# Optimization experiments

Hardware: AMD Instinct MI355X
Metric: run time of the kernel (lower is better)

## Reference

```python
import jax, jax.numpy as jnp
import numpy as np

B, S, H, I, E, K = 2, 1024, 768, 1536, 8, 2
CAPACITY_FACTOR = 1.5
ROUTING_TEMP = 1.0
LB_WEIGHT = 0.001


def setup_inputs() -> dict:
    key = jax.random.key(0)
    k_x, k_g, k_w1, k_w3, k_w2 = jax.random.split(key, 5)
    std = 0.02
    return {
        "x": jax.random.normal(k_x, (B, S, H), dtype=jnp.float32),
        "w_gate": jax.random.normal(k_g, (H, E), dtype=jnp.float32) * 0.02,
        "w1": jax.random.normal(k_w1, (E, H, I), dtype=jnp.float32) * std,
        "w3": jax.random.normal(k_w3, (E, H, I), dtype=jnp.float32) * std,
        "w2": jax.random.normal(k_w2, (E, I, H), dtype=jnp.float32) * (std / np.sqrt(2 * 12)),
    }


def _moe_forward(x, w_gate, w1, w3, w2):
    Bb, Ss, Hh = x.shape
    T = Bb * Ss
    xf = x.reshape(T, Hh)

    # --- routing ---
    gate_logits = (xf @ w_gate) / ROUTING_TEMP          # [T, E]
    gate_probs = jax.nn.softmax(gate_logits, axis=-1)   # [T, E]
    topk_probs, topk_idx = jax.lax.top_k(gate_probs, K)  # [T, K]
    topk_probs = topk_probs / (topk_probs.sum(-1, keepdims=True) + 1e-8)

    # --- capacity dropping (per-k slot, token order, like the torch loop) ---
    capacity = max(8, int((T * K // E) * CAPACITY_FACTOR))
    onehot = (topk_idx[:, :, None] == jnp.arange(E)[None, None, :])  # [T, K, E] bool
    ranks = jnp.cumsum(onehot.astype(jnp.int32), axis=0)             # position of token in expert queue
    keep = onehot & (ranks <= capacity)                               # [T, K, E]

    # combine weight per (token, expert): sum over k of kept, clamped routing prob
    w_clamped = jnp.clip(topk_probs, 1e-8, 10.0)                      # [T, K]
    combine = jnp.einsum("tk,tke->te", w_clamped, keep.astype(xf.dtype))  # [T, E]

    # --- dense per-expert SwiGLU (reference form of masked dispatch) ---
    g = jnp.einsum("th,ehi->tei", xf, w1)   # [T, E, I]
    u = jnp.einsum("th,ehi->tei", xf, w3)   # [T, E, I]
    h = jax.nn.silu(g) * u                    # [T, E, I]
    y = jnp.einsum("tei,eih->teh", h, w2)   # [T, E, H]
    out = jnp.einsum("te,teh->th", combine, y).reshape(Bb, Ss, Hh)

    # --- load balancing loss ---
    expert_counts = keep.sum(axis=(0, 1)).astype(jnp.float32)         # [E]
    dropped = (onehot.sum() - keep.sum()).astype(jnp.float32)
    expert_usage = jax.lax.stop_gradient(expert_counts) / float(max(T * K, 1))
    gate_importance = gate_probs.mean(axis=0)                          # [E]
    aux = jnp.sum(expert_usage * gate_importance) * E
    aux = aux + jnp.where(dropped > 0, dropped / float(max(T, 1)) * 0.1, 0.0)
    aux = jnp.minimum(aux, 1.0) * LB_WEIGHT
    return out, aux


def reference(x, w_gate, w1, w3, w2):
    return _moe_forward(x, w_gate, w1, w3, w2)
```

## Files before the change

### kernel.cpp

```cpp
#include <hip/hip_runtime.h>
#include <math.h>

#define T_TOK 2048
#define HD 768
#define ID 1536
#define NE 8
#define CAP 768
#define TK 4096
#define RT 12
#define NB1 24
#define KC1 24
#define NB2 12
#define KC2 48

typedef __bf16 bf16_t;
typedef __bf16 bf16x8 __attribute__((ext_vector_type(8)));
typedef __bf16 bf16x4 __attribute__((ext_vector_type(4)));
typedef float floatx4 __attribute__((ext_vector_type(4)));

__device__ __forceinline__ void gld16(const bf16_t* g, bf16_t* l) {
  __builtin_amdgcn_global_load_lds(
      (__attribute__((address_space(1))) void*)(g),
      (__attribute__((address_space(3))) void*)(l),
      16, 0, 0);
}

__global__ void k_prep(const float* __restrict__ x, const float* __restrict__ wg,
                       const float* __restrict__ w1, const float* __restrict__ w3,
                       const float* __restrict__ w2,
                       bf16_t* __restrict__ xbf, bf16_t* __restrict__ w1b,
                       bf16_t* __restrict__ w3b, bf16_t* __restrict__ w2b,
                       int2* __restrict__ idx2, float2* __restrict__ wc2,
                       float* __restrict__ probs8, float* __restrict__ outz) {
  int b = blockIdx.x;
  int tid = threadIdx.x;
  if (b < 512) {
#pragma unroll
    for (int k2 = 0; k2 < 3; ++k2) {
      float4 z = make_float4(0.f, 0.f, 0.f, 0.f);
      *(float4*)(outz + (size_t)b * 3072 + k2 * 1024 + tid * 4) = z;
    }
    int t = b * 4 + (tid >> 6);
    int lane = tid & 63;
    const float* xr = x + (size_t)t * HD;
    int off = lane * 12;
    float4 a = *(const float4*)(xr + off);
    float4 bv = *(const float4*)(xr + off + 4);
    float4 c = *(const float4*)(xr + off + 8);
    float xv[12] = {a.x, a.y, a.z, a.w, bv.x, bv.y, bv.z, bv.w, c.x, c.y, c.z, c.w};
    bf16x4 s0, s1, s2;
#pragma unroll
    for (int j = 0; j < 4; ++j) { s0[j] = (bf16_t)xv[j]; s1[j] = (bf16_t)xv[4 + j]; s2[j] = (bf16_t)xv[8 + j]; }
    bf16_t* xo = xbf + (size_t)t * HD + off;
    *(bf16x4*)xo = s0; *(bf16x4*)(xo + 4) = s1; *(bf16x4*)(xo + 8) = s2;

    float acc[8] = {0, 0, 0, 0, 0, 0, 0, 0};
#pragma unroll
    for (int jj = 0; jj < 12; ++jj) {
      const float4* wr = (const float4*)(wg + (size_t)(off + jj) * 8);
      float4 w0 = wr[0], w1v = wr[1];
      float v = xv[jj];
      acc[0] += v * w0.x; acc[1] += v * w0.y; acc[2] += v * w0.z; acc[3] += v * w0.w;
      acc[4] += v * w1v.x; acc[5] += v * w1v.y; acc[6] += v * w1v.z; acc[7] += v * w1v.w;
    }
#pragma unroll
    for (int e = 0; e < 8; ++e) {
      float v = acc[e];
      for (int s = 1; s < 64; s <<= 1) v += __shfl_xor(v, s, 64);
      acc[e] = v;
    }
    float mx = acc[0];
#pragma unroll
    for (int e = 1; e < 8; ++e) mx = fmaxf(mx, acc[e]);
    float p[8], sum = 0.f;
#pragma unroll
    for (int e = 0; e < 8; ++e) { p[e] = __expf(acc[e] - mx); sum += p[e]; }
#pragma unroll
    for (int e = 0; e < 8; ++e) p[e] /= sum;
    if (lane == 0) {
      float4 P0 = make_float4(p[0], p[1], p[2], p[3]);
      float4 P1 = make_float4(p[4], p[5], p[6], p[7]);
      *(float4*)&probs8[t * 8] = P0;
      *(float4*)&probs8[t * 8 + 4] = P1;
      int e0 = 0;
#pragma unroll
      for (int e = 1; e < 8; ++e) if (p[e] > p[e0]) e0 = e;
      int e1 = (e0 == 0) ? 1 : 0;
#pragma unroll
      for (int e = 0; e < 8; ++e) if (e != e0 && p[e] > p[e1]) e1 = e;
      float denom = p[e0] + p[e1] + 1e-8f;
      float w0c = fminf(fmaxf(p[e0] / denom, 1e-8f), 10.f);
      float w1c = fminf(fmaxf(p[e1] / denom, 1e-8f), 10.f);
      idx2[t] = make_int2(e0, e1);
      wc2[t] = make_float2(w0c, w1c);
    }
  } else {
    int rb = b - 512;
    const float* src; bf16_t* dst; int C; int kc0;
    if (rb < 1152) {
      int m = rb >= 576;
      int r3 = m ? rb - 576 : rb;
      int pan = r3 / 3;
      kc0 = (r3 - pan * 3) * 8;
      int e = pan & 7, nb = pan >> 3;
      src = (m ? w3 : w1) + (size_t)e * HD * ID + nb * 64;
      dst = (m ? w3b : w1b) + (size_t)(e * NB1 + nb) * (KC1 * 2048);
      C = ID;
    } else {
      int q = rb - 1152;
      int pan = q / 6;
      kc0 = (q - pan * 6) * 8;
      int e = pan & 7, nb = pan >> 3;
      src = w2 + (size_t)e * ID * HD + nb * 64;
      dst = w2b + (size_t)(e * NB2 + nb) * (KC2 * 2048);
      C = HD;
    }
    int n = tid >> 2, p4 = tid & 3;
    int c8 = p4 ^ ((n >> 1) & 3);
    const float* sp0 = src + n + (size_t)(kc0 * 32 + c8 * 8) * C;
    bf16_t* dp = dst + (size_t)kc0 * 2048 + tid * 8;
#pragma unroll 2
    for (int t = 0; t < 8; ++t) {
      const float* sp = sp0 + (size_t)t * 32 * C;
      float v[8];
#pragma unroll
      for (int j = 0; j < 8; ++j) v[j] = sp[(size_t)j * C];
      bf16x8 o;
#pragma unroll
      for (int j = 0; j < 8; ++j) o[j] = (bf16_t)v[j];
      *(bf16x8*)(dp + t * 2048) = o;
    }
  }
}

__global__ void k_scan(const int2* __restrict__ idx2, const float2* __restrict__ wc2,
                       const float* __restrict__ probs8,
                       int* __restrict__ tok_of_row, float* __restrict__ wgt_of_row,
                       int2* __restrict__ cnt_start, float* __restrict__ aux_out) {
  __shared__ int2 sIdx[2048];
  __shared__ float2 sWc[2048];
  __shared__ int sTot[16];
  __shared__ int sPos[8];
  __shared__ float sImp[16][8];
  int tid = threadIdx.x;
  sIdx[tid] = idx2[tid]; sIdx[tid + 1024] = idx2[tid + 1024];
  sWc[tid] = wc2[tid];  sWc[tid + 1024] = wc2[tid + 1024];
  const float4* pp = (const float4*)probs8;
  float4 u0 = pp[tid * 4], u1 = pp[tid * 4 + 1], u2 = pp[tid * 4 + 2], u3 = pp[tid * 4 + 3];
  float im[8] = {u0.x + u2.x, u0.y + u2.y, u0.z + u2.z, u0.w + u2.w,
                 u1.x + u3.x, u1.y + u3.y, u1.z + u3.z, u1.w + u3.w};
#pragma unroll
  for (int e = 0; e < 8; ++e) {
    float v = im[e];
    for (int d = 1; d < 64; d <<= 1) v += __shfl_xor(v, d, 64);
    im[e] = v;
  }
  int w = tid >> 6, lane = tid & 63;
  if (lane == 0) {
#pragma unroll
    for (int e = 0; e < 8; ++e) sImp[w][e] = im[e];
  }
  __syncthreads();
  int s = w >> 3, e = w & 7;
  int t0 = lane * 32;
  int cnt = 0;
  for (int j = 0; j < 32; ++j) {
    int2 p = sIdx[t0 + j];
    cnt += ((s ? p.y : p.x) == e) ? 1 : 0;
  }
  int incl = cnt;
  for (int d = 1; d < 64; d <<= 1) {
    int v = __shfl_up(incl, d, 64);
    if (lane >= d) incl += v;
  }
  int excl = incl - cnt;
  if (lane == 63) sTot[w] = incl;
  __syncthreads();
  if (tid == 0) {
    int run = 0; float a = 0.f;
    for (int ee = 0; ee < 8; ++ee) {
      float impv = 0.f;
      for (int ww = 0; ww < 16; ++ww) impv += sImp[ww][ee];
      int k = min(sTot[ee], CAP) + min(sTot[8 + ee], CAP);
      sPos[ee] = run;
      cnt_start[ee] = make_int2(run, k);
      a += ((float)k / (float)TK) * (impv / (float)T_TOK);
      run += k;
    }
    a *= (float)NE;
    int dropped = TK - run;
    if (dropped > 0) a += (float)dropped / (float)T_TOK * 0.1f;
    aux_out[0] = fminf(a, 1.f) * 0.001f;
  }
  __syncthreads();
  int rank = excl;
  for (int j = 0; j < 32; ++j) {
    int t = t0 + j;
    int2 p = sIdx[t];
    int ex = s ? p.y : p.x;
    if (ex == e) {
      rank++;
      if (rank <= CAP) {
        int pos = atomicAdd(&sPos[e], 1);
        tok_of_row[pos] = t;
        float2 wv = sWc[t];
        wgt_of_row[pos] = s ? wv.y : wv.x;
      }
    }
  }
}

__global__ __launch_bounds__(256, 4)
void k_gemm1(const bf16_t* __restrict__ xbf, const bf16_t* __restrict__ w1b,
             const bf16_t* __restrict__ w3b, const int* __restrict__ tok_of_row,
             const int2* __restrict__ cnt_start, bf16_t* __restrict__ h_ws) {
  int e = blockIdx.x & 7;
  int t = blockIdx.x >> 3;
  int nb = t / RT, rt = t - nb * RT;
  int2 cs = cnt_start[e];
  int nrows = cs.y - rt * 128;
  if (nrows <= 0) return;
  if (nrows > 128) nrows = 128;
  int grow0 = cs.x + rt * 128;

  __shared__ __attribute__((aligned(16))) bf16_t Abuf[128 * 32];
  __shared__ __attribute__((aligned(16))) bf16_t B1buf[64 * 32];
  __shared__ __attribute__((aligned(16))) bf16_t B3buf[64 * 32];

  int tid = threadIdx.x;
  int lane = tid & 63, wv = tid >> 6;
  int wm = wv & 1, wn = wv >> 1;
  int lr = lane & 15, q = lane >> 4;
  int rdc = (q ^ ((lane >> 1) & 3)) * 8;
  int srow = lane >> 2;
  int gch = ((lane & 3) ^ ((lane >> 3) & 3)) * 8;

  int ra = wv * 32 + srow;
  int tokA0 = tok_of_row[grow0 + min(ra, nrows - 1)];
  int tokA1 = tok_of_row[grow0 + min(ra + 16, nrows - 1)];
  const bf16_t* gA0 = xbf + (size_t)tokA0 * HD + gch;
  const bf16_t* gA1 = xbf + (size_t)tokA1 * HD + gch;
  const bf16_t* p1 = w1b + (size_t)((e * NB1 + nb) * KC1) * 2048 + tid * 8;
  const bf16_t* p3 = w3b + (size_t)((e * NB1 + nb) * KC1) * 2048 + tid * 8;
  bf16_t* lA0 = &Abuf[(wv * 32) * 32];
  bf16_t* lA1 = &Abuf[(wv * 32 + 16) * 32];
  bf16_t* lB1 = &B1buf[wv * 512];
  bf16_t* lB3 = &B3buf[wv * 512];

  floatx4 accg[4][2] = {};
  floatx4 accu[4][2] = {};

  for (int kk = 0; kk < KC1; ++kk) {
    __syncthreads();
    gld16(gA0, lA0); gld16(gA1, lA1);
    gld16(p1, lB1); gld16(p3, lB3);
    gA0 += 32; gA1 += 32; p1 += 2048; p3 += 2048;
    __syncthreads();
    bf16x8 af[4], b1f[2], b3f[2];
#pragma unroll
    for (int i = 0; i < 4; ++i) af[i] = *(const bf16x8*)&Abuf[(wm * 64 + i * 16 + lr) * 32 + rdc];
#pragma unroll
    for (int i = 0; i < 2; ++i) b1f[i] = *(const bf16x8*)&B1buf[(wn * 32 + i * 16 + lr) * 32 + rdc];
#pragma unroll
    for (int i = 0; i < 2; ++i) b3f[i] = *(const bf16x8*)&B3buf[(wn * 32 + i * 16 + lr) * 32 + rdc];
#pragma unroll
    for (int i = 0; i < 4; ++i)
#pragma unroll
      for (int jj = 0; jj < 2; ++jj) {
        accg[i][jj] = __builtin_amdgcn_mfma_f32_16x16x32_bf16(af[i], b1f[jj], accg[i][jj], 0, 0, 0);
        accu[i][jj] = __builtin_amdgcn_mfma_f32_16x16x32_bf16(af[i], b3f[jj], accu[i][jj], 0, 0, 0);
      }
  }
#pragma unroll
  for (int i = 0; i < 4; ++i)
#pragma unroll
    for (int r = 0; r < 4; ++r) {
      int rl = wm * 64 + i * 16 + q * 4 + r;
      if (rl < nrows) {
        size_t rb = (size_t)(grow0 + rl) * ID + nb * 64 + wn * 32 + lr;
#pragma unroll
        for (int jj = 0; jj < 2; ++jj) {
          float gg = accg[i][jj][r], uu = accu[i][jj][r];
          float sg = gg / (1.f + __expf(-gg));
          h_ws[rb + jj * 16] = (bf16_t)(sg * uu);
        }
      }
    }
}

__global__ __launch_bounds__(256, 4)
void k_gemm2(const bf16_t* __restrict__ h_ws, const bf16_t* __restrict__ w2b,
             const int* __restrict__ tok_of_row, const float* __restrict__ wgt_of_row,
             const int2* __restrict__ cnt_start, float* __restrict__ out) {
  int e = blockIdx.x & 7;
  int t = blockIdx.x >> 3;
  int nb = t / RT, rt = t - nb * RT;
  int2 cs = cnt_start[e];
  int nrows = cs.y - rt * 128;
  if (nrows <= 0) return;
  if (nrows > 128) nrows = 128;
  int grow0 = cs.x + rt * 128;

  __shared__ __attribute__((aligned(16))) bf16_t Abuf[128 * 32];
  __shared__ __attribute__((aligned(16))) bf16_t Bbuf[64 * 32];

  int tid = threadIdx.x;
  int lane = tid & 63, wv = tid >> 6;
  int wm = wv & 1, wn = wv >> 1;
  int lr = lane & 15, q = lane >> 4;
  int rdc = (q ^ ((lane >> 1) & 3)) * 8;
  int srow = lane >> 2;
  int gch = ((lane & 3) ^ ((lane >> 3) & 3)) * 8;

  int ra = wv * 32 + srow;
  const bf16_t* gA0 = h_ws + (size_t)(grow0 + min(ra, nrows - 1)) * ID + gch;
  const bf16_t* gA1 = h_ws + (size_t)(grow0 + min(ra + 16, nrows - 1)) * ID + gch;
  const bf16_t* pB = w2b + (size_t)((e * NB2 + nb) * KC2) * 2048 + tid * 8;
  bf16_t* lA0 = &Abuf[(wv * 32) * 32];
  bf16_t* lA1 = &Abuf[(wv * 32 + 16) * 32];
  bf16_t* lB = &Bbuf[wv * 512];

  floatx4 acc[4][2] = {};

  for (int kk = 0; kk < KC2; ++kk) {
    __syncthreads();
    gld16(gA0, lA0); gld16(gA1, lA1);
    gld16(pB, lB);
    gA0 += 32; gA1 += 32; pB += 2048;
    __syncthreads();
    bf16x8 af[4], bfr[2];
#pragma unroll
    for (int i = 0; i < 4; ++i) af[i] = *(const bf16x8*)&Abuf[(wm * 64 + i * 16 + lr) * 32 + rdc];
#pragma unroll
    for (int i = 0; i < 2; ++i) bfr[i] = *(const bf16x8*)&Bbuf[(wn * 32 + i * 16 + lr) * 32 + rdc];
#pragma unroll
    for (int i = 0; i < 4; ++i)
#pragma unroll
      for (int jj = 0; jj < 2; ++jj)
        acc[i][jj] = __builtin_amdgcn_mfma_f32_16x16x32_bf16(af[i], bfr[jj], acc[i][jj], 0, 0, 0);
  }
#pragma unroll
  for (int i = 0; i < 4; ++i)
#pragma unroll
    for (int r = 0; r < 4; ++r) {
      int rl = wm * 64 + i * 16 + q * 4 + r;
      if (rl < nrows) {
        int grow = grow0 + rl;
        int tok = tok_of_row[grow];
        float wgt = wgt_of_row[grow];
        size_t ob = (size_t)tok * HD + nb * 64 + wn * 32 + lr;
#pragma unroll
        for (int jj = 0; jj < 2; ++jj)
          atomicAdd(&out[ob + jj * 16], wgt * acc[i][jj][r]);
      }
    }
}

extern "C" void kernel_launch(void* const* d_in, const int* in_sizes, int n_in,
                              void* d_out, int out_size, void* d_ws, size_t ws_size,
                              hipStream_t stream) {
  const float* x  = (const float*)d_in[0];
  const float* wg = (const float*)d_in[1];
  const float* w1 = (const float*)d_in[2];
  const float* w3 = (const float*)d_in[3];
  const float* w2 = (const float*)d_in[4];
  float* out = (float*)d_out;

  char* ws = (char*)d_ws;
  bf16_t* xbf  = (bf16_t*)(ws + 0);
  bf16_t* w1b  = (bf16_t*)(ws + 3145728);
  bf16_t* w3b  = (bf16_t*)(ws + 22020096);
  bf16_t* w2b  = (bf16_t*)(ws + 40894464);
  bf16_t* h_ws = (bf16_t*)(ws + 59768832);
  float*  probs8     = (float*)(ws + 72351744);
  int2*   idx2       = (int2*)(ws + 72417280);
  float2* wc2        = (float2*)(ws + 72433664);
  int*    tok_of_row = (int*)(ws + 72450048);
  float*  wgt_of_row = (float*)(ws + 72466432);
  int2*   cnt_start  = (int2*)(ws + 72482816);

  float* aux_out = out + (size_t)T_TOK * HD;

  k_prep<<<2240, 256, 0, stream>>>(x, wg, w1, w3, w2, xbf, w1b, w3b, w2b,
                                   idx2, wc2, probs8, out);
  k_scan<<<1, 1024, 0, stream>>>(idx2, wc2, probs8, tok_of_row, wgt_of_row,
                                 cnt_start, aux_out);
  k_gemm1<<<8 * NB1 * RT, 256, 0, stream>>>(xbf, w1b, w3b, tok_of_row,
                                            cnt_start, h_ws);
  k_gemm2<<<8 * NB2 * RT, 256, 0, stream>>>(h_ws, w2b, tok_of_row, wgt_of_row,
                                            cnt_start, out);
}
```

Before: 261.8 us.

## Overlap weight repacking with scan and gemm1, replace atomic scatter with combine kernel

```diff
diff --git a/kernel.cpp b/kernel.cpp
--- a/kernel.cpp
+++ b/kernel.cpp
@@ -12,6 +12,7 @@
 #define KC1 24
 #define NB2 12
 #define KC2 48
+#define W2BLK 576
 
 typedef __bf16 bf16_t;
 typedef __bf16 bf16x8 __attribute__((ext_vector_type(8)));
@@ -25,126 +26,135 @@
       16, 0, 0);
 }
 
-__global__ void k_prep(const float* __restrict__ x, const float* __restrict__ wg,
-                       const float* __restrict__ w1, const float* __restrict__ w3,
-                       const float* __restrict__ w2,
-                       bf16_t* __restrict__ xbf, bf16_t* __restrict__ w1b,
-                       bf16_t* __restrict__ w3b, bf16_t* __restrict__ w2b,
-                       int2* __restrict__ idx2, float2* __restrict__ wc2,
-                       float* __restrict__ probs8, float* __restrict__ outz) {
+__device__ __forceinline__ void repack_unit256(const float* __restrict__ src,
+                                               bf16_t* __restrict__ dst, int C,
+                                               int kc0, int tid) {
+  int n = tid >> 2, p4 = tid & 3;
+  int c8 = p4 ^ ((n >> 1) & 3);
+  const float* sp0 = src + n + (size_t)(kc0 * 32 + c8 * 8) * C;
+  bf16_t* dp = dst + (size_t)kc0 * 2048 + tid * 8;
+#pragma unroll 2
+  for (int t = 0; t < 8; ++t) {
+    const float* sp = sp0 + (size_t)t * 32 * C;
+    float v[8];
+#pragma unroll
+    for (int j = 0; j < 8; ++j) v[j] = sp[(size_t)j * C];
+    bf16x8 o;
+#pragma unroll
+    for (int j = 0; j < 8; ++j) o[j] = (bf16_t)v[j];
+    *(bf16x8*)(dp + t * 2048) = o;
+  }
+}
+
+__device__ __forceinline__ void repack_unit1024(const float* __restrict__ src,
+                                                bf16_t* __restrict__ dst, int C,
+                                                int kc0, int tid1024) {
+  int tid = tid1024 & 255;
+  int tq = tid1024 >> 8;
+  int n = tid >> 2, p4 = tid & 3;
+  int c8 = p4 ^ ((n >> 1) & 3);
+  const float* sp0 = src + n + (size_t)(kc0 * 32 + c8 * 8) * C;
+  bf16_t* dp = dst + (size_t)kc0 * 2048 + tid * 8;
+#pragma unroll
+  for (int tt = 0; tt < 2; ++tt) {
+    int t = tq * 2 + tt;
+    const float* sp = sp0 + (size_t)t * 32 * C;
+    float v[8];
+#pragma unroll
+    for (int j = 0; j < 8; ++j) v[j] = sp[(size_t)j * C];
+    bf16x8 o;
+#pragma unroll
+    for (int j = 0; j < 8; ++j) o[j] = (bf16_t)v[j];
+    *(bf16x8*)(dp + t * 2048) = o;
+  }
+}
+
+__global__ void k_route(const float* __restrict__ x, const float* __restrict__ wg,
+                        bf16_t* __restrict__ xbf, int2* __restrict__ idx2,
+                        float2* __restrict__ wc2, float* __restrict__ probs8) {
   int b = blockIdx.x;
   int tid = threadIdx.x;
-  if (b < 512) {
-#pragma unroll
-    for (int k2 = 0; k2 < 3; ++k2) {
-      float4 z = make_float4(0.f, 0.f, 0.f, 0.f);
-      *(float4*)(outz + (size_t)b * 3072 + k2 * 1024 + tid * 4) = z;
-    }
-    int t = b * 4 + (tid >> 6);
-    int lane = tid & 63;
-    const float* xr = x + (size_t)t * HD;
-    int off = lane * 12;
-    float4 a = *(const float4*)(xr + off);
-    float4 bv = *(const float4*)(xr + off + 4);
-    float4 c = *(const float4*)(xr + off + 8);
-    float xv[12] = {a.x, a.y, a.z, a.w, bv.x, bv.y, bv.z, bv.w, c.x, c.y, c.z, c.w};
-    bf16x4 s0, s1, s2;
-#pragma unroll
-    for (int j = 0; j < 4; ++j) { s0[j] = (bf16_t)xv[j]; s1[j] = (bf16_t)xv[4 + j]; s2[j] = (bf16_t)xv[8 + j]; }
-    bf16_t* xo = xbf + (size_t)t * HD + off;
-    *(bf16x4*)xo = s0; *(bf16x4*)(xo + 4) = s1; *(bf16x4*)(xo + 8) = s2;
-
-    float acc[8] = {0, 0, 0, 0, 0, 0, 0, 0};
-#pragma unroll
-    for (int jj = 0; jj < 12; ++jj) {
-      const float4* wr = (const float4*)(wg + (size_t)(off + jj) * 8);
-      float4 w0 = wr[0], w1v = wr[1];
-      float v = xv[jj];
-      acc[0] += v * w0.x; acc[1] += v * w0.y; acc[2] += v * w0.z; acc[3] += v * w0.w;
-      acc[4] += v * w1v.x; acc[5] += v * w1v.y; acc[6] += v * w1v.z; acc[7] += v * w1v.w;
-    }
-#pragma unroll
-    for (int e = 0; e < 8; ++e) {
-      float v = acc[e];
-      for (int s = 1; s < 64; s <<= 1) v += __shfl_xor(v, s, 64);
-      acc[e] = v;
-    }
-    float mx = acc[0];
-#pragma unroll
-    for (int e = 1; e < 8; ++e) mx = fmaxf(mx, acc[e]);
-    float p[8], sum = 0.f;
-#pragma unroll
-    for (int e = 0; e < 8; ++e) { p[e] = __expf(acc[e] - mx); sum += p[e]; }
-#pragma unroll
-    for (int e = 0; e < 8; ++e) p[e] /= sum;
-    if (lane == 0) {
-      float4 P0 = make_float4(p[0], p[1], p[2], p[3]);
-      float4 P1 = make_float4(p[4], p[5], p[6], p[7]);
-      *(float4*)&probs8[t * 8] = P0;
-      *(float4*)&probs8[t * 8 + 4] = P1;
-      int e0 = 0;
-#pragma unroll
-      for (int e = 1; e < 8; ++e) if (p[e] > p[e0]) e0 = e;
-      int e1 = (e0 == 0) ? 1 : 0;
-#pragma unroll
-      for (int e = 0; e < 8; ++e) if (e != e0 && p[e] > p[e1]) e1 = e;
-      float denom = p[e0] + p[e1] + 1e-8f;
-      float w0c = fminf(fmaxf(p[e0] / denom, 1e-8f), 10.f);
-      float w1c = fminf(fmaxf(p[e1] / denom, 1e-8f), 10.f);
-      idx2[t] = make_int2(e0, e1);
-      wc2[t] = make_float2(w0c, w1c);
-    }
-  } else {
-    int rb = b - 512;
-    const float* src; bf16_t* dst; int C; int kc0;
-    if (rb < 1152) {
-      int m = rb >= 576;
-      int r3 = m ? rb - 576 : rb;
-      int pan = r3 / 3;
-      kc0 = (r3 - pan * 3) * 8;
-      int e = pan & 7, nb = pan >> 3;
-      src = (m ? w3 : w1) + (size_t)e * HD * ID + nb * 64;
-      dst = (m ? w3b : w1b) + (size_t)(e * NB1 + nb) * (KC1 * 2048);
-      C = ID;
-    } else {
-      int q = rb - 1152;
-      int pan = q / 6;
-      kc0 = (q - pan * 6) * 8;
-      int e = pan & 7, nb = pan >> 3;
-      src = w2 + (size_t)e * ID * HD + nb * 64;
-      dst = w2b + (size_t)(e * NB2 + nb) * (KC2 * 2048);
-      C = HD;
-    }
-    int n = tid >> 2, p4 = tid & 3;
-    int c8 = p4 ^ ((n >> 1) & 3);
-    const float* sp0 = src + n + (size_t)(kc0 * 32 + c8 * 8) * C;
-    bf16_t* dp = dst + (size_t)kc0 * 2048 + tid * 8;
-#pragma unroll 2
-    for (int t = 0; t < 8; ++t) {
-      const float* sp = sp0 + (size_t)t * 32 * C;
-      float v[8];
-#pragma unroll
-      for (int j = 0; j < 8; ++j) v[j] = sp[(size_t)j * C];
-      bf16x8 o;
-#pragma unroll
-      for (int j = 0; j < 8; ++j) o[j] = (bf16_t)v[j];
-      *(bf16x8*)(dp + t * 2048) = o;
-    }
+  int t = b * 4 + (tid >> 6);
+  int lane = tid & 63;
+  const float* xr = x + (size_t)t * HD;
+  int off = lane * 12;
+  float4 a = *(const float4*)(xr + off);
+  float4 bv = *(const float4*)(xr + off + 4);
+  float4 c = *(const float4*)(xr + off + 8);
+  float xv[12] = {a.x, a.y, a.z, a.w, bv.x, bv.y, bv.z, bv.w, c.x, c.y, c.z, c.w};
+  bf16x4 s0, s1, s2;
+#pragma unroll
+  for (int j = 0; j < 4; ++j) { s0[j] = (bf16_t)xv[j]; s1[j] = (bf16_t)xv[4 + j]; s2[j] = (bf16_t)xv[8 + j]; }
+  bf16_t* xo = xbf + (size_t)t * HD + off;
+  *(bf16x4*)xo = s0; *(bf16x4*)(xo + 4) = s1; *(bf16x4*)(xo + 8) = s2;
+
+  float acc[8] = {0, 0, 0, 0, 0, 0, 0, 0};
+#pragma unroll
+  for (int jj = 0; jj < 12; ++jj) {
+    const float4* wr = (const float4*)(wg + (size_t)(off + jj) * 8);
+    float4 w0 = wr[0], w1v = wr[1];
+    float v = xv[jj];
+    acc[0] += v * w0.x; acc[1] += v * w0.y; acc[2] += v * w0.z; acc[3] += v * w0.w;
+    acc[4] += v * w1v.x; acc[5] += v * w1v.y; acc[6] += v * w1v.z; acc[7] += v * w1v.w;
+  }
+#pragma unroll
+  for (int e = 0; e < 8; ++e) {
+    float v = acc[e];
+    for (int s = 1; s < 64; s <<= 1) v += __shfl_xor(v, s, 64);
+    acc[e] = v;
+  }
+  float mx = acc[0];
+#pragma unroll
+  for (int e = 1; e < 8; ++e) mx = fmaxf(mx, acc[e]);
+  float p[8], sum = 0.f;
+#pragma unroll
+  for (int e = 0; e < 8; ++e) { p[e] = __expf(acc[e] - mx); sum += p[e]; }
+#pragma unroll
+  for (int e = 0; e < 8; ++e) p[e] /= sum;
+  if (lane == 0) {
+    float4 P0 = make_float4(p[0], p[1], p[2], p[3]);
+    float4 P1 = make_float4(p[4], p[5], p[6], p[7]);
+    *(float4*)&probs8[t * 8] = P0;
+    *(float4*)&probs8[t * 8 + 4] = P1;
+    int e0 = 0;
+#pragma unroll
+    for (int e = 1; e < 8; ++e) if (p[e] > p[e0]) e0 = e;
+    int e1 = (e0 == 0) ? 1 : 0;
+#pragma unroll
+    for (int e = 0; e < 8; ++e) if (e != e0 && p[e] > p[e1]) e1 = e;
+    float denom = p[e0] + p[e1] + 1e-8f;
+    float w0c = fminf(fmaxf(p[e0] / denom, 1e-8f), 10.f);
+    float w1c = fminf(fmaxf(p[e1] / denom, 1e-8f), 10.f);
+    idx2[t] = make_int2(e0, e1);
+    wc2[t] = make_float2(w0c, w1c);
   }
 }
 
 __global__ void k_scan(const int2* __restrict__ idx2, const float2* __restrict__ wc2,
                        const float* __restrict__ probs8,
-                       int* __restrict__ tok_of_row, float* __restrict__ wgt_of_row,
+                       const float* __restrict__ w1, const float* __restrict__ w3,
+                       bf16_t* __restrict__ w1b, bf16_t* __restrict__ w3b,
+                       int* __restrict__ tok_of_row, int2* __restrict__ rows2,
                        int2* __restrict__ cnt_start, float* __restrict__ aux_out) {
+  if (blockIdx.x > 0) {
+    int rb = blockIdx.x - 1;
+    int m = rb >= 576;
+    int r3 = m ? rb - 576 : rb;
+    int pan = r3 / 3;
+    int kc0 = (r3 - pan * 3) * 8;
+    int e = pan & 7, nb = pan >> 3;
+    const float* src = (m ? w3 : w1) + (size_t)e * HD * ID + nb * 64;
+    bf16_t* dst = (m ? w3b : w1b) + (size_t)(e * NB1 + nb) * (KC1 * 2048);
+    repack_unit1024(src, dst, ID, kc0, threadIdx.x);
+    return;
+  }
   __shared__ int2 sIdx[2048];
-  __shared__ float2 sWc[2048];
   __shared__ int sTot[16];
   __shared__ int sPos[8];
   __shared__ float sImp[16][8];
   int tid = threadIdx.x;
   sIdx[tid] = idx2[tid]; sIdx[tid + 1024] = idx2[tid + 1024];
-  sWc[tid] = wc2[tid];  sWc[tid + 1024] = wc2[tid + 1024];
+  rows2[tid] = make_int2(-1, -1); rows2[tid + 1024] = make_int2(-1, -1);
   const float4* pp = (const float4*)probs8;
   float4 u0 = pp[tid * 4], u1 = pp[tid * 4 + 1], u2 = pp[tid * 4 + 2], u3 = pp[tid * 4 + 3];
   float im[8] = {u0.x + u2.x, u0.y + u2.y, u0.z + u2.z, u0.w + u2.w,
@@ -203,8 +213,7 @@
       if (rank <= CAP) {
         int pos = atomicAdd(&sPos[e], 1);
         tok_of_row[pos] = t;
-        float2 wv = sWc[t];
-        wgt_of_row[pos] = s ? wv.y : wv.x;
+        ((int*)rows2)[2 * t + s] = pos;
       }
     }
   }
@@ -212,10 +221,22 @@
 
 __global__ __launch_bounds__(256, 4)
 void k_gemm1(const bf16_t* __restrict__ xbf, const bf16_t* __restrict__ w1b,
-             const bf16_t* __restrict__ w3b, const int* __restrict__ tok_of_row,
+             const bf16_t* __restrict__ w3b, const float* __restrict__ w2,
+             bf16_t* __restrict__ w2b, const int* __restrict__ tok_of_row,
              const int2* __restrict__ cnt_start, bf16_t* __restrict__ h_ws) {
-  int e = blockIdx.x & 7;
-  int t = blockIdx.x >> 3;
+  if (blockIdx.x < W2BLK) {
+    int q = blockIdx.x;
+    int pan = q / 6;
+    int kc0 = (q - pan * 6) * 8;
+    int e = pan & 7, nb = pan >> 3;
+    const float* src = w2 + (size_t)e * ID * HD + nb * 64;
+    bf16_t* dst = w2b + (size_t)(e * NB2 + nb) * (KC2 * 2048);
+    repack_unit256(src, dst, HD, kc0, threadIdx.x);
+    return;
+  }
+  int bx = blockIdx.x - W2BLK;
+  int e = bx & 7;
+  int t = bx >> 3;
   int nb = t / RT, rt = t - nb * RT;
   int2 cs = cnt_start[e];
   int nrows = cs.y - rt * 128;
@@ -290,8 +311,7 @@
 
 __global__ __launch_bounds__(256, 4)
 void k_gemm2(const bf16_t* __restrict__ h_ws, const bf16_t* __restrict__ w2b,
-             const int* __restrict__ tok_of_row, const float* __restrict__ wgt_of_row,
-             const int2* __restrict__ cnt_start, float* __restrict__ out) {
+             const int2* __restrict__ cnt_start, float* __restrict__ y) {
   int e = blockIdx.x & 7;
   int t = blockIdx.x >> 3;
   int nb = t / RT, rt = t - nb * RT;
@@ -345,15 +365,41 @@
     for (int r = 0; r < 4; ++r) {
       int rl = wm * 64 + i * 16 + q * 4 + r;
       if (rl < nrows) {
-        int grow = grow0 + rl;
-        int tok = tok_of_row[grow];
-        float wgt = wgt_of_row[grow];
-        size_t ob = (size_t)tok * HD + nb * 64 + wn * 32 + lr;
+        size_t ob = (size_t)(grow0 + rl) * HD + nb * 64 + wn * 32 + lr;
 #pragma unroll
         for (int jj = 0; jj < 2; ++jj)
-          atomicAdd(&out[ob + jj * 16], wgt * acc[i][jj][r]);
+          y[ob + jj * 16] = acc[i][jj][r];
       }
     }
+}
+
+__global__ void k_comb(const float* __restrict__ y, const int2* __restrict__ rows2,
+                       const float2* __restrict__ wc2, float* __restrict__ out) {
+  int tid = threadIdx.x;
+  int t = blockIdx.x * 4 + (tid >> 6);
+  int lane = tid & 63;
+  int2 r = rows2[t];
+  float2 w = wc2[t];
+  int off = lane * 12;
+  floatx4 o0 = {0.f, 0.f, 0.f, 0.f}, o1 = o0, o2 = o0;
+  if (r.x >= 0) {
+    const float* yr = y + (size_t)r.x * HD + off;
+    floatx4 a = *(const floatx4*)(yr);
+    floatx4 b = *(const floatx4*)(yr + 4);
+    floatx4 c = *(const floatx4*)(yr + 8);
+    o0 += w.x * a; o1 += w.x * b; o2 += w.x * c;
+  }
+  if (r.y >= 0) {
+    const float* yr = y + (size_t)r.y * HD + off;
+    floatx4 a = *(const floatx4*)(yr);
+    floatx4 b = *(const floatx4*)(yr + 4);
+    floatx4 c = *(const floatx4*)(yr + 8);
+    o0 += w.y * a; o1 += w.y * b; o2 += w.y * c;
+  }
+  float* op = out + (size_t)t * HD + off;
+  *(floatx4*)(op) = o0;
+  *(floatx4*)(op + 4) = o1;
+  *(floatx4*)(op + 8) = o2;
 }
 
 extern "C" void kernel_launch(void* const* d_in, const int* in_sizes, int n_in,
@@ -376,17 +422,17 @@
   int2*   idx2       = (int2*)(ws + 72417280);
   float2* wc2        = (float2*)(ws + 72433664);
   int*    tok_of_row = (int*)(ws + 72450048);
-  float*  wgt_of_row = (float*)(ws + 72466432);
+  int2*   rows2      = (int2*)(ws + 72466432);
   int2*   cnt_start  = (int2*)(ws + 72482816);
+  float*  y_ws = (float*)(ws + 3145728);
 
   float* aux_out = out + (size_t)T_TOK * HD;
 
-  k_prep<<<2240, 256, 0, stream>>>(x, wg, w1, w3, w2, xbf, w1b, w3b, w2b,
-                                   idx2, wc2, probs8, out);
-  k_scan<<<1, 1024, 0, stream>>>(idx2, wc2, probs8, tok_of_row, wgt_of_row,
-                                 cnt_start, aux_out);
-  k_gemm1<<<8 * NB1 * RT, 256, 0, stream>>>(xbf, w1b, w3b, tok_of_row,
-                                            cnt_start, h_ws);
-  k_gemm2<<<8 * NB2 * RT, 256, 0, stream>>>(h_ws, w2b, tok_of_row, wgt_of_row,
-                                            cnt_start, out);
-}
+  k_route<<<512, 256, 0, stream>>>(x, wg, xbf, idx2, wc2, probs8);
+  k_scan<<<1 + 1152, 1024, 0, stream>>>(idx2, wc2, probs8, w1, w3, w1b, w3b,
+                                        tok_of_row, rows2, cnt_start, aux_out);
+  k_gemm1<<<W2BLK + 8 * NB1 * RT, 256, 0, stream>>>(xbf, w1b, w3b, w2, w2b,
+                                                    tok_of_row, cnt_start, h_ws);
+  k_gemm2<<<8 * NB2 * RT, 256, 0, stream>>>(h_ws, w2b, cnt_start, y_ws);
+  k_comb<<<512, 256, 0, stream>>>(y_ws, rows2, wc2, out);
+}
```

Result: faster. 235.5 us (-10.1%).

## Coalesce weight repack via LDS transpose and fuse routing scan into GEMM1

Applied to the files above, without the earlier changes.

```diff
diff --git a/kernel.cpp b/kernel.cpp
--- a/kernel.cpp
+++ b/kernel.cpp
@@ -25,16 +25,68 @@
       16, 0, 0);
 }
 
+__device__ __forceinline__ unsigned short bfbits(float f) {
+  union { bf16_t b; unsigned short u; } c;
+  c.b = (bf16_t)f;
+  return c.u;
+}
+
+__device__ __forceinline__ void rp_load(const float* __restrict__ src, int C,
+                                        int kc, int t256, unsigned* T32) {
+  int r = t256 >> 3, c0 = (t256 & 7) * 8;
+  const float* sp = src + (size_t)(kc * 32 + r) * C + c0;
+  float4 v0 = *(const float4*)sp;
+  float4 v1 = *(const float4*)(sp + 4);
+  float f[8] = {v0.x, v0.y, v0.z, v0.w, v1.x, v1.y, v1.z, v1.w};
+  unsigned* tb = T32 + r * 33 + (c0 >> 1);
+#pragma unroll
+  for (int k = 0; k < 4; ++k)
+    tb[k] = (unsigned)bfbits(f[2 * k]) | ((unsigned)bfbits(f[2 * k + 1]) << 16);
+}
+
+__device__ __forceinline__ void rp_store(bf16_t* __restrict__ dst, int kc,
+                                         int t256, const unsigned* T32) {
+  int n = t256 >> 2, p4 = t256 & 3;
+  int c8 = p4 ^ ((n >> 1) & 3);
+  int half = n & 1, nh = n >> 1;
+  unsigned short u[8];
+#pragma unroll
+  for (int j = 0; j < 8; ++j) {
+    unsigned w = T32[(c8 * 8 + j) * 33 + nh];
+    u[j] = half ? (unsigned short)(w >> 16) : (unsigned short)(w & 0xffffu);
+  }
+  uint4 o;
+  o.x = (unsigned)u[0] | ((unsigned)u[1] << 16);
+  o.y = (unsigned)u[2] | ((unsigned)u[3] << 16);
+  o.z = (unsigned)u[4] | ((unsigned)u[5] << 16);
+  o.w = (unsigned)u[6] | ((unsigned)u[7] << 16);
+  *(uint4*)(dst + (size_t)kc * 2048 + t256 * 8) = o;
+}
+
+__device__ __forceinline__ void repack8(const float* __restrict__ src,
+                                        bf16_t* __restrict__ dst, int C,
+                                        int kc0, int tid, unsigned* Trp) {
+  rp_load(src, C, kc0, tid, Trp);
+  for (int t = 0; t < 8; ++t) {
+    __syncthreads();
+    if (t < 7) rp_load(src, C, kc0 + t + 1, tid, Trp + ((t + 1) & 1) * 1056);
+    rp_store(dst, kc0 + t, tid, Trp + (t & 1) * 1056);
+  }
+}
+
 __global__ void k_prep(const float* __restrict__ x, const float* __restrict__ wg,
                        const float* __restrict__ w1, const float* __restrict__ w3,
                        const float* __restrict__ w2,
                        bf16_t* __restrict__ xbf, bf16_t* __restrict__ w1b,
                        bf16_t* __restrict__ w3b, bf16_t* __restrict__ w2b,
                        int2* __restrict__ idx2, float2* __restrict__ wc2,
-                       float* __restrict__ probs8, float* __restrict__ outz) {
+                       float* __restrict__ probs8, float* __restrict__ outz,
+                       int* __restrict__ flag) {
+  __shared__ unsigned Trp[2 * 1056];
   int b = blockIdx.x;
   int tid = threadIdx.x;
   if (b < 512) {
+    if (b == 0 && tid == 0) *flag = 0;
 #pragma unroll
     for (int k2 = 0; k2 < 3; ++k2) {
       float4 z = make_float4(0.f, 0.f, 0.f, 0.f);
@@ -94,128 +146,137 @@
       idx2[t] = make_int2(e0, e1);
       wc2[t] = make_float2(w0c, w1c);
     }
+  } else if (b < 1664) {
+    int rb = b - 512;
+    int m = rb >= 576;
+    int r3 = m ? rb - 576 : rb;
+    int pan = r3 / 3;
+    int kc0 = (r3 - pan * 3) * 8;
+    int e = pan & 7, nb = pan >> 3;
+    const float* src = (m ? w3 : w1) + (size_t)e * HD * ID + nb * 64;
+    bf16_t* dst = (m ? w3b : w1b) + (size_t)(e * NB1 + nb) * (KC1 * 2048);
+    repack8(src, dst, ID, kc0, tid, Trp);
   } else {
-    int rb = b - 512;
-    const float* src; bf16_t* dst; int C; int kc0;
-    if (rb < 1152) {
-      int m = rb >= 576;
-      int r3 = m ? rb - 576 : rb;
-      int pan = r3 / 3;
-      kc0 = (r3 - pan * 3) * 8;
-      int e = pan & 7, nb = pan >> 3;
-      src = (m ? w3 : w1) + (size_t)e * HD * ID + nb * 64;
-      dst = (m ? w3b : w1b) + (size_t)(e * NB1 + nb) * (KC1 * 2048);
-      C = ID;
-    } else {
-      int q = rb - 1152;
-      int pan = q / 6;
-      kc0 = (q - pan * 6) * 8;
-      int e = pan & 7, nb = pan >> 3;
-      src = w2 + (size_t)e * ID * HD + nb * 64;
-      dst = w2b + (size_t)(e * NB2 + nb) * (KC2 * 2048);
-      C = HD;
-    }
-    int n = tid >> 2, p4 = tid & 3;
-    int c8 = p4 ^ ((n >> 1) & 3);
-    const float* sp0 = src + n + (size_t)(kc0 * 32 + c8 * 8) * C;
-    bf16_t* dp = dst + (size_t)kc0 * 2048 + tid * 8;
-#pragma unroll 2
-    for (int t = 0; t < 8; ++t) {
-      const float* sp = sp0 + (size_t)t * 32 * C;
-      float v[8];
-#pragma unroll
-      for (int j = 0; j < 8; ++j) v[j] = sp[(size_t)j * C];
-      bf16x8 o;
-#pragma unroll
-      for (int j = 0; j < 8; ++j) o[j] = (bf16_t)v[j];
-      *(bf16x8*)(dp + t * 2048) = o;
-    }
-  }
-}
-
-__global__ void k_scan(const int2* __restrict__ idx2, const float2* __restrict__ wc2,
-                       const float* __restrict__ probs8,
-                       int* __restrict__ tok_of_row, float* __restrict__ wgt_of_row,
-                       int2* __restrict__ cnt_start, float* __restrict__ aux_out) {
-  __shared__ int2 sIdx[2048];
-  __shared__ float2 sWc[2048];
-  __shared__ int sTot[16];
-  __shared__ int sPos[8];
-  __shared__ float sImp[16][8];
+    int q = b - 1664;
+    int pan = q / 6;
+    int kc0 = (q - pan * 6) * 8;
+    int e = pan & 7, nb = pan >> 3;
+    const float* src = w2 + (size_t)e * ID * HD + nb * 64;
+    bf16_t* dst = w2b + (size_t)(e * NB2 + nb) * (KC2 * 2048);
+    repack8(src, dst, HD, kc0, tid, Trp);
+  }
+}
+
+union __attribute__((aligned(16))) SMemG1 {
+  struct { bf16_t A[128 * 32]; bf16_t B1[64 * 32]; bf16_t B3[64 * 32]; } g;
+  struct { int2 sIdx[2048]; int sTot[16]; int sPos[8]; float sImp[4][8]; } s;
+};
+
+__global__ __launch_bounds__(256, 4)
+void k_g1(const bf16_t* __restrict__ xbf, const bf16_t* __restrict__ w1b,
+          const bf16_t* __restrict__ w3b, const int2* __restrict__ idx2,
+          const float2* __restrict__ wc2, const float* __restrict__ probs8,
+          int* __restrict__ tok_of_row, float* __restrict__ wgt_of_row,
+          int2* __restrict__ cnt_start, float* __restrict__ aux_out,
+          bf16_t* __restrict__ h_ws, int* __restrict__ flag) {
+  __shared__ SMemG1 sm;
   int tid = threadIdx.x;
-  sIdx[tid] = idx2[tid]; sIdx[tid + 1024] = idx2[tid + 1024];
-  sWc[tid] = wc2[tid];  sWc[tid + 1024] = wc2[tid + 1024];
-  const float4* pp = (const float4*)probs8;
-  float4 u0 = pp[tid * 4], u1 = pp[tid * 4 + 1], u2 = pp[tid * 4 + 2], u3 = pp[tid * 4 + 3];
-  float im[8] = {u0.x + u2.x, u0.y + u2.y, u0.z + u2.z, u0.w + u2.w,
-                 u1.x + u3.x, u1.y + u3.y, u1.z + u3.z, u1.w + u3.w};
-#pragma unroll
-  for (int e = 0; e < 8; ++e) {
-    float v = im[e];
-    for (int d = 1; d < 64; d <<= 1) v += __shfl_xor(v, d, 64);
-    im[e] = v;
-  }
-  int w = tid >> 6, lane = tid & 63;
-  if (lane == 0) {
-#pragma unroll
-    for (int e = 0; e < 8; ++e) sImp[w][e] = im[e];
+  if (blockIdx.x == 0) {
+    int2* sIdx = sm.s.sIdx;
+#pragma unroll
+    for (int k = 0; k < 8; ++k) sIdx[tid + 256 * k] = idx2[tid + 256 * k];
+    const float4* pp = (const float4*)probs8;
+    float im[8] = {0, 0, 0, 0, 0, 0, 0, 0};
+#pragma unroll
+    for (int k = 0; k < 4; ++k) {
+      int T = tid + 256 * k;
+      float4 u0 = pp[T * 4], u1 = pp[T * 4 + 1], u2 = pp[T * 4 + 2], u3 = pp[T * 4 + 3];
+      im[0] += u0.x + u2.x; im[1] += u0.y + u2.y; im[2] += u0.z + u2.z; im[3] += u0.w + u2.w;
+      im[4] += u1.x + u3.x; im[5] += u1.y + u3.y; im[6] += u1.z + u3.z; im[7] += u1.w + u3.w;
+    }
+#pragma unroll
+    for (int e = 0; e < 8; ++e) {
+      float v = im[e];
+      for (int d = 1; d < 64; d <<= 1) v += __shfl_xor(v, d, 64);
+      im[e] = v;
+    }
+    int w = tid >> 6, lane = tid & 63;
+    if (lane == 0) {
+#pragma unroll
+      for (int e = 0; e < 8; ++e) sm.s.sImp[w][e] = im[e];
+    }
+    __syncthreads();
+    int t0 = lane * 32;
+    int excl4[4];
+#pragma unroll
+    for (int sub = 0; sub < 4; ++sub) {
+      int pair = w * 4 + sub;
+      int s = pair >> 3, e = pair & 7;
+      int cnt = 0;
+      for (int j = 0; j < 32; ++j) {
+        int2 p = sIdx[t0 + j];
+        cnt += ((s ? p.y : p.x) == e) ? 1 : 0;
+      }
+      int incl = cnt;
+      for (int d = 1; d < 64; d <<= 1) {
+        int v = __shfl_up(incl, d, 64);
+        if (lane >= d) incl += v;
+      }
+      excl4[sub] = incl - cnt;
+      if (lane == 63) sm.s.sTot[pair] = incl;
+    }
+    __syncthreads();
+    if (tid == 0) {
+      int run = 0; float a = 0.f;
+      for (int ee = 0; ee < 8; ++ee) {
+        float impv = sm.s.sImp[0][ee] + sm.s.sImp[1][ee] + sm.s.sImp[2][ee] + sm.s.sImp[3][ee];
+        int k = min(sm.s.sTot[ee], CAP) + min(sm.s.sTot[8 + ee], CAP);
+        sm.s.sPos[ee] = run;
+        cnt_start[ee] = make_int2(run, k);
+        a += ((float)k / (float)TK) * (impv / (float)T_TOK);
+        run += k;
+      }
+      a *= (float)NE;
+      int dropped = TK - run;
+      if (dropped > 0) a += (float)dropped / (float)T_TOK * 0.1f;
+      aux_out[0] = fminf(a, 1.f) * 0.001f;
+    }
+    __syncthreads();
+#pragma unroll
+    for (int sub = 0; sub < 4; ++sub) {
+      int pair = w * 4 + sub;
+      int s = pair >> 3, e = pair & 7;
+      int rank = excl4[sub];
+      for (int j = 0; j < 32; ++j) {
+        int t = t0 + j;
+        int2 p = sIdx[t];
+        int ex = s ? p.y : p.x;
+        if (ex == e) {
+          rank++;
+          if (rank <= CAP) {
+            int pos = atomicAdd(&sm.s.sPos[e], 1);
+            tok_of_row[pos] = t;
+            float2 wv = wc2[t];
+            wgt_of_row[pos] = s ? wv.y : wv.x;
+          }
+        }
+      }
+    }
+    __threadfence();
+    __syncthreads();
+    if (tid == 0)
+      __hip_atomic_store(flag, 1, __ATOMIC_RELEASE, __HIP_MEMORY_SCOPE_AGENT);
+    return;
+  }
+  if (tid == 0) {
+    while (__hip_atomic_load(flag, __ATOMIC_ACQUIRE, __HIP_MEMORY_SCOPE_AGENT) == 0)
+      __builtin_amdgcn_s_sleep(8);
   }
   __syncthreads();
-  int s = w >> 3, e = w & 7;
-  int t0 = lane * 32;
-  int cnt = 0;
-  for (int j = 0; j < 32; ++j) {
-    int2 p = sIdx[t0 + j];
-    cnt += ((s ? p.y : p.x) == e) ? 1 : 0;
-  }
-  int incl = cnt;
-  for (int d = 1; d < 64; d <<= 1) {
-    int v = __shfl_up(incl, d, 64);
-    if (lane >= d) incl += v;
-  }
-  int excl = incl - cnt;
-  if (lane == 63) sTot[w] = incl;
-  __syncthreads();
-  if (tid == 0) {
-    int run = 0; float a = 0.f;
-    for (int ee = 0; ee < 8; ++ee) {
-      float impv = 0.f;
-      for (int ww = 0; ww < 16; ++ww) impv += sImp[ww][ee];
-      int k = min(sTot[ee], CAP) + min(sTot[8 + ee], CAP);
-      sPos[ee] = run;
-      cnt_start[ee] = make_int2(run, k);
-      a += ((float)k / (float)TK) * (impv / (float)T_TOK);
-      run += k;
-    }
-    a *= (float)NE;
-    int dropped = TK - run;
-    if (dropped > 0) a += (float)dropped / (float)T_TOK * 0.1f;
-    aux_out[0] = fminf(a, 1.f) * 0.001f;
-  }
-  __syncthreads();
-  int rank = excl;
-  for (int j = 0; j < 32; ++j) {
-    int t = t0 + j;
-    int2 p = sIdx[t];
-    int ex = s ? p.y : p.x;
-    if (ex == e) {
-      rank++;
-      if (rank <= CAP) {
-        int pos = atomicAdd(&sPos[e], 1);
-        tok_of_row[pos] = t;
-        float2 wv = sWc[t];
-        wgt_of_row[pos] = s ? wv.y : wv.x;
-      }
-    }
-  }
-}
-
-__global__ __launch_bounds__(256, 4)
-void k_gemm1(const bf16_t* __restrict__ xbf, const bf16_t* __restrict__ w1b,
-             const bf16_t* __restrict__ w3b, const int* __restrict__ tok_of_row,
-             const int2* __restrict__ cnt_start, bf16_t* __restrict__ h_ws) {
-  int e = blockIdx.x & 7;
-  int t = blockIdx.x >> 3;
+
+  int bx = blockIdx.x - 1;
+  int e = bx & 7;
+  int t = bx >> 3;
   int nb = t / RT, rt = t - nb * RT;
   int2 cs = cnt_start[e];
   int nrows = cs.y - rt * 128;
@@ -223,11 +284,6 @@
   if (nrows > 128) nrows = 128;
   int grow0 = cs.x + rt * 128;
 
-  __shared__ __attribute__((aligned(16))) bf16_t Abuf[128 * 32];
-  __shared__ __attribute__((aligned(16))) bf16_t B1buf[64 * 32];
-  __shared__ __attribute__((aligned(16))) bf16_t B3buf[64 * 32];
-
-  int tid = threadIdx.x;
   int lane = tid & 63, wv = tid >> 6;
   int wm = wv & 1, wn = wv >> 1;
   int lr = lane & 15, q = lane >> 4;
@@ -242,10 +298,10 @@
   const bf16_t* gA1 = xbf + (size_t)tokA1 * HD + gch;
   const bf16_t* p1 = w1b + (size_t)((e * NB1 + nb) * KC1) * 2048 + tid * 8;
   const bf16_t* p3 = w3b + (size_t)((e * NB1 + nb) * KC1) * 2048 + tid * 8;
-  bf16_t* lA0 = &Abuf[(wv * 32) * 32];
-  bf16_t* lA1 = &Abuf[(wv * 32 + 16) * 32];
-  bf16_t* lB1 = &B1buf[wv * 512];
-  bf16_t* lB3 = &B3buf[wv * 512];
+  bf16_t* lA0 = &sm.g.A[(wv * 32) * 32];
+  bf16_t* lA1 = &sm.g.A[(wv * 32 + 16) * 32];
+  bf16_t* lB1 = &sm.g.B1[wv * 512];
+  bf16_t* lB3 = &sm.g.B3[wv * 512];
 
   floatx4 accg[4][2] = {};
   floatx4 accu[4][2] = {};
@@ -258,11 +314,11 @@
     __syncthreads();
     bf16x8 af[4], b1f[2], b3f[2];
 #pragma unroll
-    for (int i = 0; i < 4; ++i) af[i] = *(const bf16x8*)&Abuf[(wm * 64 + i * 16 + lr) * 32 + rdc];
-#pragma unroll
-    for (int i = 0; i < 2; ++i) b1f[i] = *(const bf16x8*)&B1buf[(wn * 32 + i * 16 + lr) * 32 + rdc];
-#pragma unroll
-    for (int i = 0; i < 2; ++i) b3f[i] = *(const bf16x8*)&B3buf[(wn * 32 + i * 16 + lr) * 32 + rdc];
+    for (int i = 0; i < 4; ++i) af[i] = *(const bf16x8*)&sm.g.A[(wm * 64 + i * 16 + lr) * 32 + rdc];
+#pragma unroll
+    for (int i = 0; i < 2; ++i) b1f[i] = *(const bf16x8*)&sm.g.B1[(wn * 32 + i * 16 + lr) * 32 + rdc];
+#pragma unroll
+    for (int i = 0; i < 2; ++i) b3f[i] = *(const bf16x8*)&sm.g.B3[(wn * 32 + i * 16 + lr) * 32 + rdc];
 #pragma unroll
     for (int i = 0; i < 4; ++i)
 #pragma unroll
@@ -289,9 +345,9 @@
 }
 
 __global__ __launch_bounds__(256, 4)
-void k_gemm2(const bf16_t* __restrict__ h_ws, const bf16_t* __restrict__ w2b,
-             const int* __restrict__ tok_of_row, const float* __restrict__ wgt_of_row,
-             const int2* __restrict__ cnt_start, float* __restrict__ out) {
+void k_g2(const bf16_t* __restrict__ h_ws, const bf16_t* __restrict__ w2b,
+          const int* __restrict__ tok_of_row, const float* __restrict__ wgt_of_row,
+          const int2* __restrict__ cnt_start, float* __restrict__ out) {
   int e = blockIdx.x & 7;
   int t = blockIdx.x >> 3;
   int nb = t / RT, rt = t - nb * RT;
@@ -378,15 +434,15 @@
   int*    tok_of_row = (int*)(ws + 72450048);
   float*  wgt_of_row = (float*)(ws + 72466432);
   int2*   cnt_start  = (int2*)(ws + 72482816);
+  int*    flag       = (int*)(ws + 72482880);
 
   float* aux_out = out + (size_t)T_TOK * HD;
 
   k_prep<<<2240, 256, 0, stream>>>(x, wg, w1, w3, w2, xbf, w1b, w3b, w2b,
-                                   idx2, wc2, probs8, out);
-  k_scan<<<1, 1024, 0, stream>>>(idx2, wc2, probs8, tok_of_row, wgt_of_row,
-                                 cnt_start, aux_out);
-  k_gemm1<<<8 * NB1 * RT, 256, 0, stream>>>(xbf, w1b, w3b, tok_of_row,
-                                            cnt_start, h_ws);
-  k_gemm2<<<8 * NB2 * RT, 256, 0, stream>>>(h_ws, w2b, tok_of_row, wgt_of_row,
-                                            cnt_start, out);
-}
+                                   idx2, wc2, probs8, out, flag);
+  k_g1<<<1 + 8 * NB1 * RT, 256, 0, stream>>>(xbf, w1b, w3b, idx2, wc2, probs8,
+                                             tok_of_row, wgt_of_row, cnt_start,
+                                             aux_out, h_ws, flag);
+  k_g2<<<8 * NB2 * RT, 256, 0, stream>>>(h_ws, w2b, tok_of_row, wgt_of_row,
+                                         cnt_start, out);
+}
```

Result: slower. 917.6 us (+250.5%).
